# Optimization experiments

Measured on AMD Instinct MI355X. Metric: run time of the kernel, lower is better.

Reference implementation:

```python
import jax, jax.numpy as jnp
import numpy as np

NUM_HEADS = 8
WS = 8
NORM_FAC = 1.0 / 200.0


def _sine_pe(coords, dim):
    # coords: [P, 2] with channels (x, y); FlowFormer LinearPositionEmbeddingSine
    nf = dim // 4
    freq = jnp.arange(nf, dtype=jnp.float32)  # linspace(0, nf-1, nf)
    px = 3.14 * coords[..., 0:1] * freq * NORM_FAC
    py = 3.14 * coords[..., 1:2] * freq * NORM_FAC
    return jnp.concatenate([jnp.sin(px), jnp.cos(px), jnp.sin(py), jnp.cos(py)], axis=-1)


def setup_inputs() -> dict:
    key = jax.random.key(0)
    ks = jax.random.split(key, 10)
    B, H, W, C = 8, 128, 128, 256
    x = jax.random.normal(ks[0], (B, H * W, C), dtype=jnp.float32)
    wscale = 0.05
    inp = {"x": x}
    for i, nm in enumerate(["q", "k", "v", "p"]):
        inp[f"W_{nm}"] = jax.random.normal(ks[1 + 2 * i], (C, C), dtype=jnp.float32) * wscale
        inp[f"b_{nm}"] = jax.random.normal(ks[2 + 2 * i], (C,), dtype=jnp.float32) * wscale
    inp["H"] = H
    inp["W"] = W
    return inp


def reference(x, W_q, b_q, W_k, b_k, W_v, b_v, W_p, b_p, H, W):
    B, N, C = x.shape
    nh, ws = NUM_HEADS, WS
    hd = C // nh
    scale = hd ** -0.5
    xg = x.reshape(B, H, W, C)
    pad_b = (-H) % ws
    pad_r = (-W) % ws
    xg = jnp.pad(xg, ((0, 0), (0, pad_b), (0, pad_r), (0, 0)))
    Hp, Wp = H + pad_b, W + pad_r
    h, w = Hp // ws, Wp // ws
    # [B, h, w, ws, ws, C] windows
    xw = xg.reshape(B, h, ws, w, ws, C).transpose(0, 1, 3, 2, 4, 5)
    # v is computed BEFORE adding the positional encoding (as in the original)
    v = xw @ W_v.T + b_v
    # sinusoidal RPE on window coordinates (same for every window)
    ys, xs = jnp.meshgrid(jnp.arange(ws, dtype=jnp.float32), jnp.arange(ws, dtype=jnp.float32), indexing="ij")
    coords = jnp.stack([xs, ys], axis=-1).reshape(-1, 2)  # [ws*ws, 2] (x, y)
    pe = _sine_pe(coords, C).reshape(ws, ws, C)
    xw = xw + pe[None, None, None]
    q = xw @ W_q.T + b_q
    k = xw @ W_k.T + b_k

    def to_heads(t):  # -> [B, h*w, nh, ws*ws, hd]
        return t.reshape(B, h * w, ws * ws, nh, hd).transpose(0, 1, 3, 2, 4)

    q, k, v = to_heads(q), to_heads(k), to_heads(v)
    attn = jax.nn.softmax(jnp.einsum("bgnpd,bgnqd->bgnpq", q, k) * scale, axis=-1)
    o = jnp.einsum("bgnpq,bgnqd->bgnpd", attn, v)
    o = o.transpose(0, 1, 3, 2, 4).reshape(B, h, w, ws, ws, C)
    o = o.transpose(0, 1, 3, 2, 4, 5).reshape(B, Hp, Wp, C)[:, :H, :W]
    return o.reshape(B, N, C) @ W_p.T + b_p
```

## Files before the change

### kernel.cpp

```cpp
#include <hip/hip_runtime.h>

typedef __bf16 bf16x8 __attribute__((ext_vector_type(8)));
typedef float f32x4 __attribute__((ext_vector_type(4)));

#define MFMA16(a, b, c) __builtin_amdgcn_mfma_f32_16x16x32_bf16((a), (b), (c), 0, 0, 0)

__device__ __forceinline__ unsigned short f2bf(float f) {
    union { float f; unsigned int u; } v;
    v.f = f;
    unsigned int r = v.u + 0x7fffu + ((v.u >> 16) & 1u);
    return (unsigned short)(r >> 16);
}

__global__ __launch_bounds__(256) void prep(
    const float* __restrict__ Wq, const float* __restrict__ bq,
    const float* __restrict__ Wk, const float* __restrict__ bk,
    const float* __restrict__ Wv, const float* __restrict__ Wp,
    unsigned short* __restrict__ Wbf,
    float* __restrict__ qpeT, float* __restrict__ kpeT)
{
    const int tid = threadIdx.x;
    {
        int i = blockIdx.x * 256 + tid;
        Wbf[i]          = f2bf(Wq[i]);
        Wbf[65536 + i]  = f2bf(Wk[i]);
        Wbf[131072 + i] = f2bf(Wv[i]);
        Wbf[196608 + i] = f2bf(Wp[i]);
    }
    if (blockIdx.x >= 64) return;

    __shared__ float pet[8 * 264];
    for (int t = tid; t < 8 * 256; t += 256) {
        int v = t >> 8, k = t & 255;
        float ang = 3.14f * (float)v * (float)(k & 63) * 0.005f;
        pet[v * 264 + k] = (k & 64) ? __cosf(ang) : __sinf(ang);
    }
    __syncthreads();

    const int p = tid & 63;
    const int c = blockIdx.x * 4 + (tid >> 6);
    const int jx = p & 7, iy = p >> 3;
    const float4* rq4 = (const float4*)(Wq + (size_t)c * 256);
    const float4* rk4 = (const float4*)(Wk + (size_t)c * 256);
    const float4* pl4 = (const float4*)(pet + jx * 264);
    const float4* ph4 = (const float4*)(pet + iy * 264);
    float aq = bq[c], ak = bk[c];
    #pragma unroll 8
    for (int t = 0; t < 32; ++t) {
        float4 pv = pl4[t], wq = rq4[t], wk = rk4[t];
        aq += pv.x * wq.x + pv.y * wq.y + pv.z * wq.z + pv.w * wq.w;
        ak += pv.x * wk.x + pv.y * wk.y + pv.z * wk.z + pv.w * wk.w;
    }
    #pragma unroll 8
    for (int t = 0; t < 32; ++t) {
        float4 pv = ph4[t], wq = rq4[32 + t], wk = rk4[32 + t];
        aq += pv.x * wq.x + pv.y * wq.y + pv.z * wq.z + pv.w * wq.w;
        ak += pv.x * wk.x + pv.y * wk.y + pv.z * wk.z + pv.w * wk.w;
    }
    qpeT[c * 64 + p] = aq;
    kpeT[c * 64 + p] = ak;
}

#define STRX 264
#define STRV 72
#define VSOFF 16896

__global__ __launch_bounds__(512, 4) void fused_attn(
    const float* __restrict__ x,
    const unsigned short* __restrict__ Wall,
    const float* __restrict__ bv,
    const float* __restrict__ qpeT,
    const float* __restrict__ kpeT,
    const float* __restrict__ bp,
    float* __restrict__ out)
{
    __shared__ unsigned short sm[35328];
    unsigned short* xs = sm;
    unsigned short* vs = sm + VSOFF;
    unsigned short* os = sm + VSOFF;

    const int tid  = threadIdx.x;
    const int w    = tid >> 6;
    const int lane = tid & 63;
    const int quad = lane >> 4;
    const int l15  = lane & 15;

    const int g = blockIdx.x;
    const int b = g >> 8, wy = (g >> 4) & 15, wx = g & 15;
    const int rowbase = b * 16384 + wy * 1024 + wx * 8;

    const f32x4 zero4 = {0.f, 0.f, 0.f, 0.f};

    {
        const int tk = tid >> 3;
        const int c0 = (tid & 7) * 32;
        const int gr = rowbase + (tk >> 3) * 128 + (tk & 7);
        const float* xr = x + (size_t)gr * 256 + c0;
        #pragma unroll
        for (int i = 0; i < 32; i += 8) {
            float4 f0 = *(const float4*)(xr + i);
            float4 f1 = *(const float4*)(xr + i + 4);
            alignas(16) unsigned short st[8] = {
                f2bf(f0.x), f2bf(f0.y), f2bf(f0.z), f2bf(f0.w),
                f2bf(f1.x), f2bf(f1.y), f2bf(f1.z), f2bf(f1.w)};
            *(uint4*)&xs[tk * STRX + c0 + i] = *(const uint4*)st;
        }
    }
    __syncthreads();

    {
        const unsigned short* Wv = Wall + 131072;
        f32x4 acc[4][2];
        #pragma unroll
        for (int i = 0; i < 4; ++i) { acc[i][0] = zero4; acc[i][1] = zero4; }
        #pragma unroll 2
        for (int k0 = 0; k0 < 256; k0 += 32) {
            bf16x8 af[4], wv[2];
            #pragma unroll
            for (int i = 0; i < 4; ++i)
                af[i] = *(const bf16x8*)&xs[(i * 16 + l15) * STRX + k0 + quad * 8];
            #pragma unroll
            for (int j = 0; j < 2; ++j)
                wv[j] = *(const bf16x8*)&Wv[(size_t)(w * 32 + j * 16 + l15) * 256 + k0 + quad * 8];
            #pragma unroll
            for (int i = 0; i < 4; ++i)
                #pragma unroll
                for (int j = 0; j < 2; ++j)
                    acc[i][j] = MFMA16(af[i], wv[j], acc[i][j]);
        }
        #pragma unroll
        for (int j = 0; j < 2; ++j) {
            const int ch = w * 32 + j * 16 + l15;
            const float bbv = bv[ch];
            #pragma unroll
            for (int i = 0; i < 4; ++i) {
                alignas(8) unsigned short t4[4];
                #pragma unroll
                for (int r = 0; r < 4; ++r) t4[r] = f2bf(acc[i][j][r] + bbv);
                *(uint2*)&vs[ch * STRV + i * 16 + quad * 4] = *(const uint2*)t4;
            }
        }
    }

    f32x4 aq[4][2], ak[4][2];
    {
        const unsigned short* Wq = Wall;
        const unsigned short* Wk = Wall + 65536;
        #pragma unroll
        for (int i = 0; i < 4; ++i)
            #pragma unroll
            for (int j = 0; j < 2; ++j) { aq[i][j] = zero4; ak[i][j] = zero4; }
        #pragma unroll 2
        for (int k0 = 0; k0 < 256; k0 += 32) {
            bf16x8 af[4], wq[2], wk[2];
            #pragma unroll
            for (int i = 0; i < 4; ++i)
                af[i] = *(const bf16x8*)&xs[(i * 16 + l15) * STRX + k0 + quad * 8];
            #pragma unroll
            for (int j = 0; j < 2; ++j) {
                wq[j] = *(const bf16x8*)&Wq[(size_t)(w * 32 + j * 16 + l15) * 256 + k0 + quad * 8];
                wk[j] = *(const bf16x8*)&Wk[(size_t)(w * 32 + j * 16 + l15) * 256 + k0 + quad * 8];
            }
            #pragma unroll
            for (int i = 0; i < 4; ++i)
                #pragma unroll
                for (int j = 0; j < 2; ++j) {
                    aq[i][j] = MFMA16(wq[j], af[i], aq[i][j]);
                    ak[i][j] = MFMA16(wk[j], af[i], ak[i][j]);
                }
        }
    }

    f32x4 oaT[2][4];
    {
        const float* qb = qpeT + (size_t)(w * 32 + quad * 4) * 64 + l15;
        const float* kb = kpeT + (size_t)(w * 32 + quad * 4) * 64 + l15;
        bf16x8 fq[4], fk[4];
        #pragma unroll
        for (int i = 0; i < 4; ++i) {
            alignas(16) unsigned short tq[8], tk8[8];
            #pragma unroll
            for (int e = 0; e < 8; ++e) {
                const int j = e >> 2, r = e & 3;
                const int off = (j * 16 + r) * 64 + i * 16;
                tq[e]  = f2bf(aq[i][j][r] + qb[off]);
                tk8[e] = f2bf(ak[i][j][r] + kb[off]);
            }
            fq[i] = *(const bf16x8*)tq;
            fk[i] = *(const bf16x8*)tk8;
        }

        f32x4 s[4][4];
        #pragma unroll
        for (int pt = 0; pt < 4; ++pt)
            #pragma unroll
            for (int mt = 0; mt < 4; ++mt)
                s[pt][mt] = MFMA16(fk[pt], fq[mt], zero4);

        const float KF = 0.17677669529663687f * 1.4426950408889634f;
        #pragma unroll
        for (int mt = 0; mt < 4; ++mt) {
            float mx = s[0][mt][0];
            #pragma unroll
            for (int pt = 0; pt < 4; ++pt)
                #pragma unroll
                for (int r = 0; r < 4; ++r) mx = fmaxf(mx, s[pt][mt][r]);
            mx = fmaxf(mx, __shfl_xor(mx, 16));
            mx = fmaxf(mx, __shfl_xor(mx, 32));
            float sum = 0.f;
            #pragma unroll
            for (int pt = 0; pt < 4; ++pt)
                #pragma unroll
                for (int r = 0; r < 4; ++r) {
                    float e = exp2f((s[pt][mt][r] - mx) * KF);
                    s[pt][mt][r] = e;
                    sum += e;
                }
            sum += __shfl_xor(sum, 16);
            sum += __shfl_xor(sum, 32);
            const float inv = 1.0f / sum;
            #pragma unroll
            for (int pt = 0; pt < 4; ++pt)
                #pragma unroll
                for (int r = 0; r < 4; ++r) s[pt][mt][r] *= inv;
        }

        #pragma unroll
        for (int nv = 0; nv < 2; ++nv)
            #pragma unroll
            for (int mt = 0; mt < 4; ++mt) oaT[nv][mt] = zero4;
        #pragma unroll
        for (int kt = 0; kt < 2; ++kt) {
            bf16x8 pf[4], vf[2];
            #pragma unroll
            for (int mt = 0; mt < 4; ++mt) {
                alignas(16) unsigned short t8[8];
                #pragma unroll
                for (int e = 0; e < 8; ++e)
                    t8[e] = f2bf(s[kt * 2 + (e >> 2)][mt][e & 3]);
                pf[mt] = *(const bf16x8*)t8;
            }
            #pragma unroll
            for (int nv = 0; nv < 2; ++nv) {
                const int c = w * 32 + nv * 16 + l15;
                alignas(16) unsigned short t8[8];
                *(uint2*)&t8[0] = *(const uint2*)&vs[c * STRV + kt * 32 + quad * 4];
                *(uint2*)&t8[4] = *(const uint2*)&vs[c * STRV + kt * 32 + 16 + quad * 4];
                vf[nv] = *(const bf16x8*)t8;
            }
            #pragma unroll
            for (int nv = 0; nv < 2; ++nv)
                #pragma unroll
                for (int mt = 0; mt < 4; ++mt)
                    oaT[nv][mt] = MFMA16(vf[nv], pf[mt], oaT[nv][mt]);
        }
    }
    __syncthreads();

    #pragma unroll
    for (int mt = 0; mt < 4; ++mt)
        #pragma unroll
        for (int nv = 0; nv < 2; ++nv) {
            alignas(8) unsigned short t4[4];
            #pragma unroll
            for (int r = 0; r < 4; ++r) t4[r] = f2bf(oaT[nv][mt][r]);
            *(uint2*)&os[(mt * 16 + l15) * STRX + w * 32 + nv * 16 + quad * 4] = *(const uint2*)t4;
        }
    __syncthreads();

    {
        const unsigned short* Wp = Wall + 196608;
        f32x4 ac[4][2];
        #pragma unroll
        for (int i = 0; i < 4; ++i) { ac[i][0] = zero4; ac[i][1] = zero4; }
        #pragma unroll 2
        for (int k0 = 0; k0 < 256; k0 += 32) {
            bf16x8 af[4], bb[2];
            #pragma unroll
            for (int i = 0; i < 4; ++i)
                af[i] = *(const bf16x8*)&os[(i * 16 + l15) * STRX + k0 + quad * 8];
            #pragma unroll
            for (int j = 0; j < 2; ++j)
                bb[j] = *(const bf16x8*)&Wp[(size_t)(w * 32 + j * 16 + l15) * 256 + k0 + quad * 8];
            #pragma unroll
            for (int i = 0; i < 4; ++i)
                #pragma unroll
                for (int j = 0; j < 2; ++j)
                    ac[i][j] = MFMA16(af[i], bb[j], ac[i][j]);
        }
        #pragma unroll
        for (int j = 0; j < 2; ++j) {
            const int n = w * 32 + j * 16 + l15;
            const float bbp = bp[n];
            #pragma unroll
            for (int i = 0; i < 4; ++i) {
                #pragma unroll
                for (int r = 0; r < 4; ++r) {
                    const int m = i * 16 + quad * 4 + r;
                    const int gr = rowbase + (m >> 3) * 128 + (m & 7);
                    out[(size_t)gr * 256 + n] = ac[i][j][r] + bbp;
                }
            }
        }
    }
}

extern "C" void kernel_launch(void* const* d_in, const int* in_sizes, int n_in,
                              void* d_out, int out_size, void* d_ws, size_t ws_size,
                              hipStream_t stream) {
    const float* x  = (const float*)d_in[0];
    const float* Wq = (const float*)d_in[1];
    const float* bq = (const float*)d_in[2];
    const float* Wk = (const float*)d_in[3];
    const float* bk = (const float*)d_in[4];
    const float* Wv = (const float*)d_in[5];
    const float* bv = (const float*)d_in[6];
    const float* Wp = (const float*)d_in[7];
    const float* bp = (const float*)d_in[8];
    float* out = (float*)d_out;

    char* ws = (char*)d_ws;
    unsigned short* Wbf = (unsigned short*)ws;
    float* qpeT = (float*)(ws + 524288);
    float* kpeT = (float*)(ws + 524288 + 65536);

    prep<<<256, 256, 0, stream>>>(Wq, bq, Wk, bk, Wv, Wp, Wbf, qpeT, kpeT);
    fused_attn<<<2048, 512, 0, stream>>>(x, Wbf, bv, qpeT, kpeT, bp, out);
}
```

Measured before the change: 367.2 us.

## Vectorize output stores, pre-permute PE tables, use native bf16 casts and setprio

Swaps the operands of the output projection MFMA so each lane holds four consecutive channels, which lets the output be written with float4 stores instead of scalar stores. The prep kernel writes the positional q/k bias tables in a lane-contiguous permuted layout so the fused kernel reads them with float4 loads. Manual float-to-bf16 rounding is replaced by native __bf16 conversions. s_setprio brackets are added around the MFMA groups. Together these target store, load and conversion instruction overhead, at the cost of depending on the compiler's bf16 conversion rounding matching the manual routine.

Measured after the change: 391.5 us. +6.6%, slower.

```diff
diff --git a/kernel.cpp b/kernel.cpp
--- a/kernel.cpp
+++ b/kernel.cpp
@@ -1,6 +1,7 @@
 #include <hip/hip_runtime.h>
 
 typedef __bf16 bf16x8 __attribute__((ext_vector_type(8)));
+typedef __bf16 bf16x4 __attribute__((ext_vector_type(4)));
 typedef float f32x4 __attribute__((ext_vector_type(4)));
 
 #define MFMA16(a, b, c) __builtin_amdgcn_mfma_f32_16x16x32_bf16((a), (b), (c), 0, 0, 0)
@@ -17,7 +18,7 @@
     const float* __restrict__ Wk, const float* __restrict__ bk,
     const float* __restrict__ Wv, const float* __restrict__ Wp,
     unsigned short* __restrict__ Wbf,
-    float* __restrict__ qpeT, float* __restrict__ kpeT)
+    float* __restrict__ qpeP, float* __restrict__ kpeP)
 {
     const int tid = threadIdx.x;
     {
@@ -57,8 +58,12 @@
         aq += pv.x * wq.x + pv.y * wq.y + pv.z * wq.z + pv.w * wq.w;
         ak += pv.x * wk.x + pv.y * wk.y + pv.z * wk.z + pv.w * wk.w;
     }
-    qpeT[c * 64 + p] = aq;
-    kpeT[c * 64 + p] = ak;
+    const int w = c >> 5, quad = (c >> 2) & 3;
+    const int e = ((c >> 4) & 1) * 4 + (c & 3);
+    const int i = p >> 4, l15 = p & 15;
+    const int idx = ((w * 4 + quad) * 16 + l15) * 32 + i * 8 + e;
+    qpeP[idx] = aq;
+    kpeP[idx] = ak;
 }
 
 #define STRX 264
@@ -69,8 +74,8 @@
     const float* __restrict__ x,
     const unsigned short* __restrict__ Wall,
     const float* __restrict__ bv,
-    const float* __restrict__ qpeT,
-    const float* __restrict__ kpeT,
+    const float* __restrict__ qpeP,
+    const float* __restrict__ kpeP,
     const float* __restrict__ bp,
     float* __restrict__ out)
 {
@@ -100,10 +105,12 @@
         for (int i = 0; i < 32; i += 8) {
             float4 f0 = *(const float4*)(xr + i);
             float4 f1 = *(const float4*)(xr + i + 4);
-            alignas(16) unsigned short st[8] = {
-                f2bf(f0.x), f2bf(f0.y), f2bf(f0.z), f2bf(f0.w),
-                f2bf(f1.x), f2bf(f1.y), f2bf(f1.z), f2bf(f1.w)};
-            *(uint4*)&xs[tk * STRX + c0 + i] = *(const uint4*)st;
+            bf16x8 v;
+            v[0] = (__bf16)f0.x; v[1] = (__bf16)f0.y;
+            v[2] = (__bf16)f0.z; v[3] = (__bf16)f0.w;
+            v[4] = (__bf16)f1.x; v[5] = (__bf16)f1.y;
+            v[6] = (__bf16)f1.z; v[7] = (__bf16)f1.w;
+            *(bf16x8*)&xs[tk * STRX + c0 + i] = v;
         }
     }
     __syncthreads();
@@ -122,11 +129,13 @@
             #pragma unroll
             for (int j = 0; j < 2; ++j)
                 wv[j] = *(const bf16x8*)&Wv[(size_t)(w * 32 + j * 16 + l15) * 256 + k0 + quad * 8];
+            __builtin_amdgcn_s_setprio(1);
             #pragma unroll
             for (int i = 0; i < 4; ++i)
                 #pragma unroll
                 for (int j = 0; j < 2; ++j)
                     acc[i][j] = MFMA16(af[i], wv[j], acc[i][j]);
+            __builtin_amdgcn_s_setprio(0);
         }
         #pragma unroll
         for (int j = 0; j < 2; ++j) {
@@ -134,10 +143,10 @@
             const float bbv = bv[ch];
             #pragma unroll
             for (int i = 0; i < 4; ++i) {
-                alignas(8) unsigned short t4[4];
-                #pragma unroll
-                for (int r = 0; r < 4; ++r) t4[r] = f2bf(acc[i][j][r] + bbv);
-                *(uint2*)&vs[ch * STRV + i * 16 + quad * 4] = *(const uint2*)t4;
+                bf16x4 t;
+                #pragma unroll
+                for (int r = 0; r < 4; ++r) t[r] = (__bf16)(acc[i][j][r] + bbv);
+                *(bf16x4*)&vs[ch * STRV + i * 16 + quad * 4] = t;
             }
         }
     }
@@ -161,6 +170,7 @@
                 wq[j] = *(const bf16x8*)&Wq[(size_t)(w * 32 + j * 16 + l15) * 256 + k0 + quad * 8];
                 wk[j] = *(const bf16x8*)&Wk[(size_t)(w * 32 + j * 16 + l15) * 256 + k0 + quad * 8];
             }
+            __builtin_amdgcn_s_setprio(1);
             #pragma unroll
             for (int i = 0; i < 4; ++i)
                 #pragma unroll
@@ -168,34 +178,41 @@
                     aq[i][j] = MFMA16(wq[j], af[i], aq[i][j]);
                     ak[i][j] = MFMA16(wk[j], af[i], ak[i][j]);
                 }
+            __builtin_amdgcn_s_setprio(0);
         }
     }
 
     f32x4 oaT[2][4];
     {
-        const float* qb = qpeT + (size_t)(w * 32 + quad * 4) * 64 + l15;
-        const float* kb = kpeT + (size_t)(w * 32 + quad * 4) * 64 + l15;
+        const float* qb = qpeP + (size_t)((w * 4 + quad) * 16 + l15) * 32;
+        const float* kb = kpeP + (size_t)((w * 4 + quad) * 16 + l15) * 32;
         bf16x8 fq[4], fk[4];
         #pragma unroll
         for (int i = 0; i < 4; ++i) {
-            alignas(16) unsigned short tq[8], tk8[8];
-            #pragma unroll
-            for (int e = 0; e < 8; ++e) {
-                const int j = e >> 2, r = e & 3;
-                const int off = (j * 16 + r) * 64 + i * 16;
-                tq[e]  = f2bf(aq[i][j][r] + qb[off]);
-                tk8[e] = f2bf(ak[i][j][r] + kb[off]);
-            }
-            fq[i] = *(const bf16x8*)tq;
-            fk[i] = *(const bf16x8*)tk8;
+            float4 q0 = *(const float4*)(qb + i * 8);
+            float4 q1 = *(const float4*)(qb + i * 8 + 4);
+            float4 k0v = *(const float4*)(kb + i * 8);
+            float4 k1v = *(const float4*)(kb + i * 8 + 4);
+            bf16x8 vq, vk;
+            vq[0] = (__bf16)(aq[i][0][0] + q0.x); vq[1] = (__bf16)(aq[i][0][1] + q0.y);
+            vq[2] = (__bf16)(aq[i][0][2] + q0.z); vq[3] = (__bf16)(aq[i][0][3] + q0.w);
+            vq[4] = (__bf16)(aq[i][1][0] + q1.x); vq[5] = (__bf16)(aq[i][1][1] + q1.y);
+            vq[6] = (__bf16)(aq[i][1][2] + q1.z); vq[7] = (__bf16)(aq[i][1][3] + q1.w);
+            vk[0] = (__bf16)(ak[i][0][0] + k0v.x); vk[1] = (__bf16)(ak[i][0][1] + k0v.y);
+            vk[2] = (__bf16)(ak[i][0][2] + k0v.z); vk[3] = (__bf16)(ak[i][0][3] + k0v.w);
+            vk[4] = (__bf16)(ak[i][1][0] + k1v.x); vk[5] = (__bf16)(ak[i][1][1] + k1v.y);
+            vk[6] = (__bf16)(ak[i][1][2] + k1v.z); vk[7] = (__bf16)(ak[i][1][3] + k1v.w);
+            fq[i] = vq; fk[i] = vk;
         }
 
         f32x4 s[4][4];
+        __builtin_amdgcn_s_setprio(1);
         #pragma unroll
         for (int pt = 0; pt < 4; ++pt)
             #pragma unroll
             for (int mt = 0; mt < 4; ++mt)
                 s[pt][mt] = MFMA16(fk[pt], fq[mt], zero4);
+        __builtin_amdgcn_s_setprio(0);
 
         const float KF = 0.17677669529663687f * 1.4426950408889634f;
         #pragma unroll
@@ -234,25 +251,26 @@
             bf16x8 pf[4], vf[2];
             #pragma unroll
             for (int mt = 0; mt < 4; ++mt) {
-                alignas(16) unsigned short t8[8];
+                bf16x8 v;
                 #pragma unroll
                 for (int e = 0; e < 8; ++e)
-                    t8[e] = f2bf(s[kt * 2 + (e >> 2)][mt][e & 3]);
-                pf[mt] = *(const bf16x8*)t8;
+                    v[e] = (__bf16)(s[kt * 2 + (e >> 2)][mt][e & 3]);
+                pf[mt] = v;
             }
             #pragma unroll
             for (int nv = 0; nv < 2; ++nv) {
                 const int c = w * 32 + nv * 16 + l15;
-                alignas(16) unsigned short t8[8];
-                *(uint2*)&t8[0] = *(const uint2*)&vs[c * STRV + kt * 32 + quad * 4];
-                *(uint2*)&t8[4] = *(const uint2*)&vs[c * STRV + kt * 32 + 16 + quad * 4];
-                vf[nv] = *(const bf16x8*)t8;
-            }
+                bf16x4 lo = *(const bf16x4*)&vs[c * STRV + kt * 32 + quad * 4];
+                bf16x4 hi = *(const bf16x4*)&vs[c * STRV + kt * 32 + 16 + quad * 4];
+                vf[nv] = __builtin_shufflevector(lo, hi, 0, 1, 2, 3, 4, 5, 6, 7);
+            }
+            __builtin_amdgcn_s_setprio(1);
             #pragma unroll
             for (int nv = 0; nv < 2; ++nv)
                 #pragma unroll
                 for (int mt = 0; mt < 4; ++mt)
                     oaT[nv][mt] = MFMA16(vf[nv], pf[mt], oaT[nv][mt]);
+            __builtin_amdgcn_s_setprio(0);
         }
     }
     __syncthreads();
@@ -261,10 +279,10 @@
     for (int mt = 0; mt < 4; ++mt)
         #pragma unroll
         for (int nv = 0; nv < 2; ++nv) {
-            alignas(8) unsigned short t4[4];
-            #pragma unroll
-            for (int r = 0; r < 4; ++r) t4[r] = f2bf(oaT[nv][mt][r]);
-            *(uint2*)&os[(mt * 16 + l15) * STRX + w * 32 + nv * 16 + quad * 4] = *(const uint2*)t4;
+            bf16x4 t;
+            #pragma unroll
+            for (int r = 0; r < 4; ++r) t[r] = (__bf16)oaT[nv][mt][r];
+            *(bf16x4*)&os[(mt * 16 + l15) * STRX + w * 32 + nv * 16 + quad * 4] = t;
         }
     __syncthreads();
 
@@ -282,24 +300,28 @@
             #pragma unroll
             for (int j = 0; j < 2; ++j)
                 bb[j] = *(const bf16x8*)&Wp[(size_t)(w * 32 + j * 16 + l15) * 256 + k0 + quad * 8];
+            __builtin_amdgcn_s_setprio(1);
             #pragma unroll
             for (int i = 0; i < 4; ++i)
                 #pragma unroll
                 for (int j = 0; j < 2; ++j)
-                    ac[i][j] = MFMA16(af[i], bb[j], ac[i][j]);
+                    ac[i][j] = MFMA16(bb[j], af[i], ac[i][j]);
+            __builtin_amdgcn_s_setprio(0);
         }
         #pragma unroll
         for (int j = 0; j < 2; ++j) {
-            const int n = w * 32 + j * 16 + l15;
-            const float bbp = bp[n];
+            const int n0 = w * 32 + j * 16 + quad * 4;
+            const float4 bpv = *(const float4*)&bp[n0];
             #pragma unroll
             for (int i = 0; i < 4; ++i) {
-                #pragma unroll
-                for (int r = 0; r < 4; ++r) {
-                    const int m = i * 16 + quad * 4 + r;
-                    const int gr = rowbase + (m >> 3) * 128 + (m & 7);
-                    out[(size_t)gr * 256 + n] = ac[i][j][r] + bbp;
-                }
+                const int tok = i * 16 + l15;
+                const int gr = rowbase + (tok >> 3) * 128 + (tok & 7);
+                float4 o4;
+                o4.x = ac[i][j][0] + bpv.x;
+                o4.y = ac[i][j][1] + bpv.y;
+                o4.z = ac[i][j][2] + bpv.z;
+                o4.w = ac[i][j][3] + bpv.w;
+                *(float4*)&out[(size_t)gr * 256 + n0] = o4;
             }
         }
     }
@@ -321,9 +343,9 @@
 
     char* ws = (char*)d_ws;
     unsigned short* Wbf = (unsigned short*)ws;
-    float* qpeT = (float*)(ws + 524288);
-    float* kpeT = (float*)(ws + 524288 + 65536);
-
-    prep<<<256, 256, 0, stream>>>(Wq, bq, Wk, bk, Wv, Wp, Wbf, qpeT, kpeT);
-    fused_attn<<<2048, 512, 0, stream>>>(x, Wbf, bv, qpeT, kpeT, bp, out);
+    float* qpeP = (float*)(ws + 524288);
+    float* kpeP = (float*)(ws + 524288 + 65536);
+
+    prep<<<256, 256, 0, stream>>>(Wq, bq, Wk, bk, Wv, Wp, Wbf, qpeP, kpeP);
+    fused_attn<<<2048, 512, 0, stream>>>(x, Wbf, bv, qpeP, kpeP, bp, out);
 }
```
